# Performance work log

Measured on AMD Instinct MI355X. Metric: run time of the kernel, lower is better.

Reference implementation:

```python
import jax, jax.numpy as jnp
import numpy as np

N_EMBED = 1024
HEAD_SIZE = 128
B, T = 4, 2048

def setup_inputs() -> dict:
    key = jax.random.key(0)
    kx, kq, kk, kv = jax.random.split(key, 4)
    bound = 1.0 / np.sqrt(N_EMBED)  # torch Linear default init range
    x = jax.random.normal(kx, (B, T, N_EMBED), dtype=jnp.float32)
    Wq = jax.random.uniform(kq, (N_EMBED, HEAD_SIZE), jnp.float32, -bound, bound)
    Wk = jax.random.uniform(kk, (N_EMBED, HEAD_SIZE), jnp.float32, -bound, bound)
    Wv = jax.random.uniform(kv, (N_EMBED, HEAD_SIZE), jnp.float32, -bound, bound)
    return {"x": x, "Wq": Wq, "Wk": Wk, "Wv": Wv}

def reference(x, Wq, Wk, Wv):
    Bn, Tn, C = x.shape
    q = x @ Wq  # [B,T,H]
    k = x @ Wk
    v = x @ Wv
    # NOTE: original scales by C**-0.5 where C = n_embed (not head_size)
    scale = C ** (-0.5)
    wei = jnp.einsum('bqh,bkh->bqk', q, k) * scale  # [B,T,T]
    causal = jnp.tril(jnp.ones((Tn, Tn), dtype=bool))
    wei = jnp.where(causal, wei, -jnp.inf)
    wei = jax.nn.softmax(wei, axis=-1)
    # dropout p=0.0 -> identity
    return jnp.einsum('bqk,bkh->bqh', wei, v)
```

## Files before the change

kernel.cpp:

```cpp
#include <hip/hip_runtime.h>
#include <stdint.h>

#define B_ 4
#define T_ 2048
#define C_ 1024
#define H_ 128
#define NEG_BIG -3.0e38f

typedef __attribute__((ext_vector_type(8))) short short8;
typedef __attribute__((ext_vector_type(4))) float f32x4;
typedef __attribute__((ext_vector_type(4))) unsigned short ushort4v;
typedef __attribute__((ext_vector_type(8))) unsigned short ushort8v;

__device__ __forceinline__ unsigned short f2bf(float f) {
  union { float f; unsigned u; } cv; cv.f = f;
  return (unsigned short)((cv.u + 0x8000u) >> 16);
}

__device__ __forceinline__ float bf2f(unsigned short s) {
  union { unsigned u; float f; } cv; cv.u = ((unsigned)s) << 16;
  return cv.f;
}

__device__ __forceinline__ void gld16(const void* g, void* l) {
  __builtin_amdgcn_global_load_lds(
      (const __attribute__((address_space(1))) unsigned int*)g,
      (__attribute__((address_space(3))) unsigned int*)l, 16, 0, 0);
}

#define CSCALE 0.045084220027780106f

__global__ __launch_bounds__(256) void prep_w(const float* __restrict__ Wq,
                                              const float* __restrict__ Wk,
                                              const float* __restrict__ Wv,
                                              unsigned short* __restrict__ WbT) {
  const int i = blockIdx.x * 256 + threadIdx.x;
  const int linear = i * 4;
  const int j = linear >> 10;
  const int k0 = linear & 1023;
  const float* W = (j < 128) ? Wq : (j < 256) ? Wk : Wv;
  const int h = j & 127;
  ushort4v p;
  p[0] = f2bf(W[(k0 + 0) * 128 + h]);
  p[1] = f2bf(W[(k0 + 1) * 128 + h]);
  p[2] = f2bf(W[(k0 + 2) * 128 + h]);
  p[3] = f2bf(W[(k0 + 3) * 128 + h]);
  *(ushort4v*)(WbT + linear) = p;
}

__global__ __launch_bounds__(256, 2) void qkv_proj(const float* __restrict__ x,
                                                   const unsigned short* __restrict__ WbT,
                                                   unsigned short* __restrict__ Qb,
                                                   unsigned short* __restrict__ Kb,
                                                   unsigned short* __restrict__ VT) {
  __shared__ unsigned short As[2][64 * 64];
  __shared__ unsigned short Bs[2][96 * 64];

  const int tid  = threadIdx.x;
  const int wave = tid >> 6, lane = tid & 63;
  const int quad = lane >> 4, l15 = lane & 15;
  const int rb = blockIdx.x & 127, cb = blockIdx.x >> 7;
  const int gm0 = rb * 64, gn0 = cb * 96;
  const int wm = wave >> 1, wn = wave & 1;

  const int srow = lane >> 3, sslot = lane & 7;
  const int axr = tid >> 3, axc = tid & 7;
  const float* gAx = x + (size_t)(gm0 + axr) * C_ + axc * 8;

  int aoff[2][2], boff[3][2];
#pragma unroll
  for (int mt = 0; mt < 2; ++mt) {
    const int r = wm * 32 + mt * 16 + l15;
#pragma unroll
    for (int ks = 0; ks < 2; ++ks)
      aoff[mt][ks] = r * 64 + (((ks * 4 + quad) ^ r) & 7) * 8;
  }
#pragma unroll
  for (int nt = 0; nt < 3; ++nt) {
    const int r = wn * 48 + nt * 16 + l15;
#pragma unroll
    for (int ks = 0; ks < 2; ++ks)
      boff[nt][ks] = r * 64 + (((ks * 4 + quad) ^ r) & 7) * 8;
  }

  f32x4 acc[2][3];
  const f32x4 zero4 = {0.f, 0.f, 0.f, 0.f};
#pragma unroll
  for (int mt = 0; mt < 2; ++mt)
#pragma unroll
    for (int nt = 0; nt < 3; ++nt) acc[mt][nt] = zero4;

#define STAGE_B(buf, kb_)                                                          \
  {                                                                                \
    const int ko = (kb_) * 64;                                                     \
    _Pragma("unroll")                                                              \
    for (int q = 0; q < 3; ++q) {                                                  \
      const int row = wave * 24 + q * 8 + srow;                                    \
      gld16(WbT + (size_t)(gn0 + row) * C_ + ko + ((sslot ^ row) & 7) * 8,         \
            &Bs[buf][(wave * 24 + q * 8) * 64]);                                   \
    }                                                                              \
  }

#define LOAD_A(ko_)                                                                \
  _Pragma("unroll")                                                                \
  for (int q = 0; q < 2; ++q) {                                                    \
    av0[q] = *(const f32x4*)(gAx + (size_t)(q * 32) * C_ + (ko_));                 \
    av1[q] = *(const f32x4*)(gAx + (size_t)(q * 32) * C_ + (ko_) + 4);             \
  }

#define WRITE_A(buf)                                                               \
  _Pragma("unroll")                                                                \
  for (int q = 0; q < 2; ++q) {                                                    \
    const int row = axr + q * 32;                                                  \
    short8 aw;                                                                     \
    _Pragma("unroll")                                                              \
    for (int e = 0; e < 4; ++e) {                                                  \
      aw[e]     = (short)f2bf(av0[q][e]);                                          \
      aw[4 + e] = (short)f2bf(av1[q][e]);                                          \
    }                                                                              \
    *(short8*)(&As[buf][row * 64 + ((axc ^ row) & 7) * 8]) = aw;                   \
  }

  f32x4 av0[2], av1[2];
  LOAD_A(0);
  STAGE_B(0, 0);
  WRITE_A(0);

  for (int kb = 0; kb < 16; ++kb) {
    __syncthreads();
    const int cur = kb & 1, nxt = cur ^ 1;
    if (kb + 1 < 16) {
      LOAD_A((kb + 1) * 64);
      STAGE_B(nxt, kb + 1);
    }
    const unsigned short* Ac = As[cur];
    const unsigned short* Bc = Bs[cur];
#pragma unroll
    for (int ks = 0; ks < 2; ++ks) {
      short8 b0 = *(const short8*)(Bc + boff[0][ks]);
      short8 b1 = *(const short8*)(Bc + boff[1][ks]);
      short8 b2 = *(const short8*)(Bc + boff[2][ks]);
#pragma unroll
      for (int mt = 0; mt < 2; ++mt) {
        short8 a = *(const short8*)(Ac + aoff[mt][ks]);
        acc[mt][0] = __builtin_amdgcn_mfma_f32_16x16x32_bf16(a, b0, acc[mt][0], 0, 0, 0);
        acc[mt][1] = __builtin_amdgcn_mfma_f32_16x16x32_bf16(a, b1, acc[mt][1], 0, 0, 0);
        acc[mt][2] = __builtin_amdgcn_mfma_f32_16x16x32_bf16(a, b2, acc[mt][2], 0, 0, 0);
      }
    }
    if (kb + 1 < 16) WRITE_A(nxt);
  }
#undef STAGE_B
#undef LOAD_A
#undef WRITE_A

#pragma unroll
  for (int mt = 0; mt < 2; ++mt) {
    const int row0 = gm0 + wm * 32 + mt * 16 + quad * 4;
#pragma unroll
    for (int nt = 0; nt < 3; ++nt) {
      const int colbase = gn0 + wn * 48 + nt * 16;
      const int col = colbase + l15;
      if (colbase < 128) {
#pragma unroll
        for (int r = 0; r < 4; ++r)
          Qb[(size_t)(row0 + r) * H_ + col] = f2bf(acc[mt][nt][r] * CSCALE);
      } else if (colbase < 256) {
#pragma unroll
        for (int r = 0; r < 4; ++r)
          Kb[(size_t)(row0 + r) * H_ + (col - 128)] = f2bf(acc[mt][nt][r]);
      } else {
        const int h = col - 256;
        const int bidx = row0 >> 11;
        const int t0 = row0 & 2047;
        ushort4v pk;
        pk[0] = f2bf(acc[mt][nt][0]); pk[1] = f2bf(acc[mt][nt][1]);
        pk[2] = f2bf(acc[mt][nt][2]); pk[3] = f2bf(acc[mt][nt][3]);
        *(ushort4v*)(VT + (size_t)(bidx * H_ + h) * T_ + t0) = pk;
      }
    }
  }
}

__global__ __launch_bounds__(256, 2) void attn1(const unsigned short* __restrict__ Qb,
                                                const unsigned short* __restrict__ Kb,
                                                const unsigned short* __restrict__ VT,
                                                unsigned short* __restrict__ Opart,
                                                float* __restrict__ mpart,
                                                float* __restrict__ lpart) {
  __shared__ unsigned short Ks[2][64 * 128];
  __shared__ unsigned short Vs[2][128 * 64];
  __shared__ unsigned short Pls[4][16 * 72];
  __shared__ float Als[4][16];

  const int bid = blockIdx.x;
  const int b  = bid & 3;
  const int jp = (bid >> 2) & 15;
  const int ch = bid >> 6;
  const int j1 = jp, j2 = 31 - jp;
  const int n1 = (ch <= j1) ? (((j1 - ch) >> 3) + 1) : 0;
  const int n2 = ((j2 - ch) >> 3) + 1;
  const int ntt = n1 + n2;

  const int tid  = threadIdx.x;
  const int wave = tid >> 6, lane = tid & 63;
  const int quad = lane >> 4, l15 = lane & 15;

  const unsigned short* Kb_b = Kb + (size_t)(b * T_) * H_;
  const unsigned short* VT_b = VT + (size_t)(b * H_) * T_;

  const int k_row4 = lane >> 4, k_slot = lane & 15;
  const int v_row8 = lane >> 3, v_slot = lane & 7;

#define STAGE_KV(buf, kv0_)                                                        \
  {                                                                                \
    _Pragma("unroll")                                                              \
    for (int i_ = 0; i_ < 4; ++i_) {                                               \
      const int r = wave * 16 + i_ * 4 + k_row4;                                   \
      const int c2 = (k_slot & 8) | ((k_slot ^ r) & 7);                            \
      gld16(Kb_b + (size_t)((kv0_) + r) * H_ + c2 * 8,                             \
            &Ks[buf][(wave * 16 + i_ * 4) * 128]);                                 \
    }                                                                              \
    _Pragma("unroll")                                                              \
    for (int i_ = 0; i_ < 4; ++i_) {                                               \
      const int h = wave * 32 + i_ * 8 + v_row8;                                   \
      gld16(VT_b + (size_t)h * T_ + (kv0_) + ((v_slot ^ h) & 7) * 8,               \
            &Vs[buf][(wave * 32 + i_ * 8) * 64]);                                  \
    }                                                                              \
  }

#define EPI(jr_)                                                                   \
  {                                                                                \
    const int pid = (b * 32 + (jr_)) * 8 + ch;                                     \
    unsigned short* po = Opart + (size_t)(pid * 64 + wave * 16) * H_;              \
    _Pragma("unroll")                                                              \
    for (int nth = 0; nth < 8; ++nth)                                              \
      _Pragma("unroll")                                                            \
      for (int r = 0; r < 4; ++r)                                                  \
        po[(quad * 4 + r) * H_ + nth * 16 + l15] = f2bf(O[nth][r]);                \
    if (lane < 16) {                                                               \
      mpart[pid * 64 + wave * 16 + lane] = m_;                                     \
      lpart[pid * 64 + wave * 16 + lane] = l_;                                     \
    }                                                                              \
  }

  int jr_cur = n1 ? j1 : j2;
  short8 aq[4];
  {
    const unsigned short* qrow = Qb + (size_t)(b * T_ + jr_cur * 64 + wave * 16 + l15) * H_;
#pragma unroll
    for (int ks = 0; ks < 4; ++ks)
      aq[ks] = *(const short8*)(qrow + ks * 32 + quad * 8);
  }

  STAGE_KV(0, ch * 64);

  const f32x4 zero4 = {0.f, 0.f, 0.f, 0.f};
  f32x4 O[8];
#pragma unroll
  for (int nth = 0; nth < 8; ++nth) O[nth] = zero4;
  float m_ = NEG_BIG, l_ = 0.f;

  for (int i = 0; i < ntt; ++i) {
    __syncthreads();
    if (i + 1 < ntt) {
      const int in_ = i + 1;
      const int tn = (in_ < n1) ? (ch + (in_ << 3)) : (ch + ((in_ - n1) << 3));
      STAGE_KV((in_) & 1, tn * 64);
    }
    if (n1 && i == n1) {
      EPI(j1);
      m_ = NEG_BIG; l_ = 0.f;
#pragma unroll
      for (int nth = 0; nth < 8; ++nth) O[nth] = zero4;
      jr_cur = j2;
      const unsigned short* qrow = Qb + (size_t)(b * T_ + j2 * 64 + wave * 16 + l15) * H_;
#pragma unroll
      for (int ks = 0; ks < 4; ++ks)
        aq[ks] = *(const short8*)(qrow + ks * 32 + quad * 8);
    }
    const int ti  = (i < n1) ? (ch + (i << 3)) : (ch + ((i - n1) << 3));
    const int kv0 = ti * 64;

    const unsigned short* kb = Ks[i & 1];
    f32x4 ST[4];
    ST[0] = zero4; ST[1] = zero4; ST[2] = zero4; ST[3] = zero4;
#pragma unroll
    for (int ntl = 0; ntl < 4; ++ntl) {
      const int kvr = ntl * 16 + l15;
#pragma unroll
      for (int ks = 0; ks < 4; ++ks) {
        const int c = ks * 4 + quad;
        const int slot = (c & 8) | ((c ^ kvr) & 7);
        short8 kf = *(const short8*)(kb + kvr * 128 + slot * 8);
        ST[ntl] = __builtin_amdgcn_mfma_f32_16x16x32_bf16(kf, aq[ks], ST[ntl], 0, 0, 0);
      }
    }

    if (ti == jr_cur) {
      const int ql = jr_cur * 64 + wave * 16 + l15;
#pragma unroll
      for (int ntl = 0; ntl < 4; ++ntl)
#pragma unroll
        for (int r = 0; r < 4; ++r) {
          const int kl = kv0 + ntl * 16 + quad * 4 + r;
          if (kl > ql) ST[ntl][r] = NEG_BIG;
        }
    }

    float vmax = ST[0][0];
#pragma unroll
    for (int ntl = 0; ntl < 4; ++ntl)
#pragma unroll
      for (int r = 0; r < 4; ++r) vmax = fmaxf(vmax, ST[ntl][r]);
    vmax = fmaxf(vmax, __shfl_xor(vmax, 16));
    vmax = fmaxf(vmax, __shfl_xor(vmax, 32));
    const float mn = fmaxf(m_, vmax);
    const float alpha = __builtin_amdgcn_exp2f(m_ - mn);
    m_ = mn;
    float s = 0.f;
#pragma unroll
    for (int ntl = 0; ntl < 4; ++ntl)
#pragma unroll
      for (int r = 0; r < 4; ++r) {
        const float p = __builtin_amdgcn_exp2f(ST[ntl][r] - mn);
        ST[ntl][r] = p;
        s += p;
      }
    s += __shfl_xor(s, 16);
    s += __shfl_xor(s, 32);
    l_ = l_ * alpha + s;

#pragma unroll
    for (int ntl = 0; ntl < 4; ++ntl) {
      ushort4v pk;
      pk[0] = f2bf(ST[ntl][0]); pk[1] = f2bf(ST[ntl][1]);
      pk[2] = f2bf(ST[ntl][2]); pk[3] = f2bf(ST[ntl][3]);
      *(ushort4v*)(&Pls[wave][l15 * 72 + ntl * 16 + quad * 4]) = pk;
    }

    if (lane < 16) Als[wave][lane] = alpha;
    if (!__all(alpha == 1.f)) {
      f32x4 al4 = *(const f32x4*)&Als[wave][quad * 4];
#pragma unroll
      for (int nth = 0; nth < 8; ++nth)
#pragma unroll
        for (int r = 0; r < 4; ++r) O[nth][r] *= al4[r];
    }

    const unsigned short* vb = Vs[i & 1];
    short8 ap0 = *(const short8*)(&Pls[wave][l15 * 72 + quad * 8]);
    short8 ap1 = *(const short8*)(&Pls[wave][l15 * 72 + 32 + quad * 8]);
#pragma unroll
    for (int nth = 0; nth < 8; ++nth) {
      const int h = nth * 16 + l15;
      short8 v0 = *(const short8*)(vb + h * 64 + ((quad ^ h) & 7) * 8);
      short8 v1 = *(const short8*)(vb + h * 64 + (((4 + quad) ^ h) & 7) * 8);
      O[nth] = __builtin_amdgcn_mfma_f32_16x16x32_bf16(ap0, v0, O[nth], 0, 0, 0);
      O[nth] = __builtin_amdgcn_mfma_f32_16x16x32_bf16(ap1, v1, O[nth], 0, 0, 0);
    }
  }
  EPI(j2);
#undef STAGE_KV
#undef EPI
}

__global__ __launch_bounds__(256) void attn2(const unsigned short* __restrict__ Opart,
                                             const float* __restrict__ mpart,
                                             const float* __restrict__ lpart,
                                             float* __restrict__ out) {
  const int b = blockIdx.x & 3;
  const int j = blockIdx.x >> 2;
  const int nch = min(j + 1, 8);
  const int tid = threadIdx.x;
  const int qh = tid >> 4;
  const int h0 = (tid & 15) * 8;
  const int pbase = (b * 32 + j) * 8;

#pragma unroll
  for (int i = 0; i < 4; ++i) {
    const int q = qh + i * 16;
    float m_fin = NEG_BIG;
    for (int ch = 0; ch < nch; ++ch)
      m_fin = fmaxf(m_fin, mpart[(pbase + ch) * 64 + q]);
    float lf = 0.f;
    float o[8];
#pragma unroll
    for (int c = 0; c < 8; ++c) o[c] = 0.f;
    for (int ch = 0; ch < nch; ++ch) {
      const int pid = pbase + ch;
      const float sc = __builtin_amdgcn_exp2f(mpart[pid * 64 + q] - m_fin);
      lf += sc * lpart[pid * 64 + q];
      ushort8v pv = *(const ushort8v*)(Opart + (size_t)(pid * 64 + q) * H_ + h0);
#pragma unroll
      for (int c = 0; c < 8; ++c) o[c] += sc * bf2f(pv[c]);
    }
    const float inv = 1.0f / lf;
    float* op = out + (size_t)(b * T_ + j * 64 + q) * H_ + h0;
    f32x4 v0 = {o[0] * inv, o[1] * inv, o[2] * inv, o[3] * inv};
    f32x4 v1 = {o[4] * inv, o[5] * inv, o[6] * inv, o[7] * inv};
    *(f32x4*)(op) = v0;
    *(f32x4*)(op + 4) = v1;
  }
}

extern "C" void kernel_launch(void* const* d_in, const int* in_sizes, int n_in,
                              void* d_out, int out_size, void* d_ws, size_t ws_size,
                              hipStream_t stream) {
  const float* x  = (const float*)d_in[0];
  const float* Wq = (const float*)d_in[1];
  const float* Wk = (const float*)d_in[2];
  const float* Wv = (const float*)d_in[3];
  float* out = (float*)d_out;

  char* ws = (char*)d_ws;
  unsigned short* WbT = (unsigned short*)(ws);
  unsigned short* Qb  = (unsigned short*)(ws + 1048576);
  unsigned short* Kb  = (unsigned short*)(ws + 3145728);
  unsigned short* VT  = (unsigned short*)(ws + 5242880);
  unsigned short* Opart = (unsigned short*)(ws + 8388608);
  float* mpart = (float*)(ws + 25165824);
  float* lpart = (float*)(ws + 25427968);

  prep_w<<<dim3(384), dim3(256), 0, stream>>>(Wq, Wk, Wv, WbT);
  qkv_proj<<<dim3(512), dim3(256), 0, stream>>>(x, WbT, Qb, Kb, VT);
  attn1<<<dim3(512), dim3(256), 0, stream>>>(Qb, Kb, VT, Opart, mpart, lpart);
  attn2<<<dim3(128), dim3(256), 0, stream>>>(Opart, mpart, lpart, out);
}
```

Baseline: 133.2 us.

## Fuse all four stages into one persistent kernel with grid barriers

Merges weight prep, QKV projection, split attention and the combine step into a single kernel of 512 blocks. Stages are separated by atomic-counter grid barriers instead of separate launches, and the counter is reset with a memset before each launch. This removes three kernel launch gaps and the tails between them. In exchange it needs all 512 blocks resident at once (2 per CU, about 75KB of shared memory each), spends time spinning at each barrier, and the combine stage is now spread over 512 blocks instead of 128.

```diff
diff --git a/kernel.cpp b/kernel.cpp
--- a/kernel.cpp
+++ b/kernel.cpp
@@ -28,358 +28,366 @@
       (__attribute__((address_space(3))) unsigned int*)l, 16, 0, 0);
 }
 
+__device__ __forceinline__ void gbar(unsigned int* cnt, unsigned int target) {
+  __threadfence();
+  __syncthreads();
+  if (threadIdx.x == 0) {
+    __hip_atomic_fetch_add(cnt, 1u, __ATOMIC_ACQ_REL, __HIP_MEMORY_SCOPE_AGENT);
+    unsigned int v;
+    do {
+      __builtin_amdgcn_s_sleep(2);
+      v = __hip_atomic_load(cnt, __ATOMIC_ACQUIRE, __HIP_MEMORY_SCOPE_AGENT);
+    } while (v < target);
+  }
+  __syncthreads();
+  __threadfence();
+}
+
 #define CSCALE 0.045084220027780106f
 
-__global__ __launch_bounds__(256) void prep_w(const float* __restrict__ Wq,
-                                              const float* __restrict__ Wk,
-                                              const float* __restrict__ Wv,
-                                              unsigned short* __restrict__ WbT) {
-  const int i = blockIdx.x * 256 + threadIdx.x;
-  const int linear = i * 4;
-  const int j = linear >> 10;
-  const int k0 = linear & 1023;
-  const float* W = (j < 128) ? Wq : (j < 256) ? Wk : Wv;
-  const int h = j & 127;
-  ushort4v p;
-  p[0] = f2bf(W[(k0 + 0) * 128 + h]);
-  p[1] = f2bf(W[(k0 + 1) * 128 + h]);
-  p[2] = f2bf(W[(k0 + 2) * 128 + h]);
-  p[3] = f2bf(W[(k0 + 3) * 128 + h]);
-  *(ushort4v*)(WbT + linear) = p;
-}
-
-__global__ __launch_bounds__(256, 2) void qkv_proj(const float* __restrict__ x,
-                                                   const unsigned short* __restrict__ WbT,
-                                                   unsigned short* __restrict__ Qb,
-                                                   unsigned short* __restrict__ Kb,
-                                                   unsigned short* __restrict__ VT) {
-  __shared__ unsigned short As[2][64 * 64];
-  __shared__ unsigned short Bs[2][96 * 64];
-
-  const int tid  = threadIdx.x;
+__global__ __launch_bounds__(256, 2) void fused_head(
+    const float* __restrict__ x, const float* __restrict__ Wq,
+    const float* __restrict__ Wk, const float* __restrict__ Wv,
+    unsigned short* __restrict__ WbT, unsigned short* __restrict__ Qb,
+    unsigned short* __restrict__ Kb, unsigned short* __restrict__ VT,
+    unsigned short* __restrict__ Opart, float* __restrict__ mpart,
+    float* __restrict__ lpart, unsigned int* __restrict__ gsync,
+    float* __restrict__ out) {
+  __shared__ __align__(16) char smem[75008];
+
+  const int tid = threadIdx.x;
+  const int bid = blockIdx.x;
   const int wave = tid >> 6, lane = tid & 63;
   const int quad = lane >> 4, l15 = lane & 15;
-  const int rb = blockIdx.x & 127, cb = blockIdx.x >> 7;
-  const int gm0 = rb * 64, gn0 = cb * 96;
-  const int wm = wave >> 1, wn = wave & 1;
-
-  const int srow = lane >> 3, sslot = lane & 7;
-  const int axr = tid >> 3, axc = tid & 7;
-  const float* gAx = x + (size_t)(gm0 + axr) * C_ + axc * 8;
-
-  int aoff[2][2], boff[3][2];
-#pragma unroll
-  for (int mt = 0; mt < 2; ++mt) {
-    const int r = wm * 32 + mt * 16 + l15;
-#pragma unroll
-    for (int ks = 0; ks < 2; ++ks)
-      aoff[mt][ks] = r * 64 + (((ks * 4 + quad) ^ r) & 7) * 8;
+
+  {
+    const int i = bid * 256 + tid;
+    if (i < 98304) {
+      const int linear = i * 4;
+      const int j = linear >> 10;
+      const int k0 = linear & 1023;
+      const float* W = (j < 128) ? Wq : (j < 256) ? Wk : Wv;
+      const int h = j & 127;
+      ushort4v p;
+      p[0] = f2bf(W[(k0 + 0) * 128 + h]);
+      p[1] = f2bf(W[(k0 + 1) * 128 + h]);
+      p[2] = f2bf(W[(k0 + 2) * 128 + h]);
+      p[3] = f2bf(W[(k0 + 3) * 128 + h]);
+      *(ushort4v*)(WbT + linear) = p;
+    }
   }
-#pragma unroll
-  for (int nt = 0; nt < 3; ++nt) {
-    const int r = wn * 48 + nt * 16 + l15;
-#pragma unroll
-    for (int ks = 0; ks < 2; ++ks)
-      boff[nt][ks] = r * 64 + (((ks * 4 + quad) ^ r) & 7) * 8;
+  gbar(gsync, 512);
+
+  {
+    unsigned short* const Asm = (unsigned short*)smem;
+    unsigned short* const Bsm = (unsigned short*)(smem + 16384);
+
+    const int rb = bid & 127, cb = bid >> 7;
+    const int gm0 = rb * 64, gn0 = cb * 96;
+    const int wm = wave >> 1, wn = wave & 1;
+    const int srow = lane >> 3, sslot = lane & 7;
+    const int axr = tid >> 3, axc = tid & 7;
+    const float* gAx = x + (size_t)(gm0 + axr) * C_ + axc * 8;
+
+    int aoff[2][2], boff[3][2];
+#pragma unroll
+    for (int mt = 0; mt < 2; ++mt) {
+      const int r = wm * 32 + mt * 16 + l15;
+#pragma unroll
+      for (int ks = 0; ks < 2; ++ks)
+        aoff[mt][ks] = r * 64 + (((ks * 4 + quad) ^ r) & 7) * 8;
+    }
+#pragma unroll
+    for (int nt = 0; nt < 3; ++nt) {
+      const int r = wn * 48 + nt * 16 + l15;
+#pragma unroll
+      for (int ks = 0; ks < 2; ++ks)
+        boff[nt][ks] = r * 64 + (((ks * 4 + quad) ^ r) & 7) * 8;
+    }
+
+    f32x4 acc[2][3];
+    const f32x4 zero4 = {0.f, 0.f, 0.f, 0.f};
+#pragma unroll
+    for (int mt = 0; mt < 2; ++mt)
+#pragma unroll
+      for (int nt = 0; nt < 3; ++nt) acc[mt][nt] = zero4;
+
+#define QSTAGE_B(buf, kb_)                                                         \
+    {                                                                              \
+      const int ko = (kb_) * 64;                                                   \
+      _Pragma("unroll")                                                            \
+      for (int q = 0; q < 3; ++q) {                                                \
+        const int row = wave * 24 + q * 8 + srow;                                  \
+        gld16(WbT + (size_t)(gn0 + row) * C_ + ko + ((sslot ^ row) & 7) * 8,       \
+              Bsm + (buf) * 6144 + (wave * 24 + q * 8) * 64);                      \
+      }                                                                            \
+    }
+
+#define QLOAD_A(ko_)                                                               \
+    _Pragma("unroll")                                                              \
+    for (int q = 0; q < 2; ++q) {                                                  \
+      av0[q] = *(const f32x4*)(gAx + (size_t)(q * 32) * C_ + (ko_));               \
+      av1[q] = *(const f32x4*)(gAx + (size_t)(q * 32) * C_ + (ko_) + 4);           \
+    }
+
+#define QWRITE_A(buf)                                                              \
+    _Pragma("unroll")                                                              \
+    for (int q = 0; q < 2; ++q) {                                                  \
+      const int row = axr + q * 32;                                                \
+      short8 aw;                                                                   \
+      _Pragma("unroll")                                                            \
+      for (int e = 0; e < 4; ++e) {                                                \
+        aw[e]     = (short)f2bf(av0[q][e]);                                        \
+        aw[4 + e] = (short)f2bf(av1[q][e]);                                        \
+      }                                                                            \
+      *(short8*)(Asm + (buf) * 4096 + row * 64 + ((axc ^ row) & 7) * 8) = aw;      \
+    }
+
+    f32x4 av0[2], av1[2];
+    QLOAD_A(0);
+    QSTAGE_B(0, 0);
+    QWRITE_A(0);
+
+    for (int kb = 0; kb < 16; ++kb) {
+      __syncthreads();
+      const int cur = kb & 1, nxt = cur ^ 1;
+      if (kb + 1 < 16) {
+        QLOAD_A((kb + 1) * 64);
+        QSTAGE_B(nxt, kb + 1);
+      }
+      const unsigned short* Ac = Asm + cur * 4096;
+      const unsigned short* Bc = Bsm + cur * 6144;
+#pragma unroll
+      for (int ks = 0; ks < 2; ++ks) {
+        short8 b0 = *(const short8*)(Bc + boff[0][ks]);
+        short8 b1 = *(const short8*)(Bc + boff[1][ks]);
+        short8 b2 = *(const short8*)(Bc + boff[2][ks]);
+#pragma unroll
+        for (int mt = 0; mt < 2; ++mt) {
+          short8 a = *(const short8*)(Ac + aoff[mt][ks]);
+          acc[mt][0] = __builtin_amdgcn_mfma_f32_16x16x32_bf16(a, b0, acc[mt][0], 0, 0, 0);
+          acc[mt][1] = __builtin_amdgcn_mfma_f32_16x16x32_bf16(a, b1, acc[mt][1], 0, 0, 0);
+          acc[mt][2] = __builtin_amdgcn_mfma_f32_16x16x32_bf16(a, b2, acc[mt][2], 0, 0, 0);
+        }
+      }
+      if (kb + 1 < 16) QWRITE_A(nxt);
+    }
+#undef QSTAGE_B
+#undef QLOAD_A
+#undef QWRITE_A
+
+#pragma unroll
+    for (int mt = 0; mt < 2; ++mt) {
+      const int row0 = gm0 + wm * 32 + mt * 16 + quad * 4;
+#pragma unroll
+      for (int nt = 0; nt < 3; ++nt) {
+        const int colbase = gn0 + wn * 48 + nt * 16;
+        const int col = colbase + l15;
+        if (colbase < 128) {
+#pragma unroll
+          for (int r = 0; r < 4; ++r)
+            Qb[(size_t)(row0 + r) * H_ + col] = f2bf(acc[mt][nt][r] * CSCALE);
+        } else if (colbase < 256) {
+#pragma unroll
+          for (int r = 0; r < 4; ++r)
+            Kb[(size_t)(row0 + r) * H_ + (col - 128)] = f2bf(acc[mt][nt][r]);
+        } else {
+          const int h = col - 256;
+          const int bidx = row0 >> 11;
+          const int t0 = row0 & 2047;
+          ushort4v pk;
+          pk[0] = f2bf(acc[mt][nt][0]); pk[1] = f2bf(acc[mt][nt][1]);
+          pk[2] = f2bf(acc[mt][nt][2]); pk[3] = f2bf(acc[mt][nt][3]);
+          *(ushort4v*)(VT + (size_t)(bidx * H_ + h) * T_ + t0) = pk;
+        }
+      }
+    }
   }
-
-  f32x4 acc[2][3];
-  const f32x4 zero4 = {0.f, 0.f, 0.f, 0.f};
-#pragma unroll
-  for (int mt = 0; mt < 2; ++mt)
-#pragma unroll
-    for (int nt = 0; nt < 3; ++nt) acc[mt][nt] = zero4;
-
-#define STAGE_B(buf, kb_)                                                          \
-  {                                                                                \
-    const int ko = (kb_) * 64;                                                     \
-    _Pragma("unroll")                                                              \
-    for (int q = 0; q < 3; ++q) {                                                  \
-      const int row = wave * 24 + q * 8 + srow;                                    \
-      gld16(WbT + (size_t)(gn0 + row) * C_ + ko + ((sslot ^ row) & 7) * 8,         \
-            &Bs[buf][(wave * 24 + q * 8) * 64]);                                   \
-    }                                                                              \
-  }
-
-#define LOAD_A(ko_)                                                                \
-  _Pragma("unroll")                                                                \
-  for (int q = 0; q < 2; ++q) {                                                    \
-    av0[q] = *(const f32x4*)(gAx + (size_t)(q * 32) * C_ + (ko_));                 \
-    av1[q] = *(const f32x4*)(gAx + (size_t)(q * 32) * C_ + (ko_) + 4);             \
-  }
-
-#define WRITE_A(buf)                                                               \
-  _Pragma("unroll")                                                                \
-  for (int q = 0; q < 2; ++q) {                                                    \
-    const int row = axr + q * 32;                                                  \
-    short8 aw;                                                                     \
-    _Pragma("unroll")                                                              \
-    for (int e = 0; e < 4; ++e) {                                                  \
-      aw[e]     = (short)f2bf(av0[q][e]);                                          \
-      aw[4 + e] = (short)f2bf(av1[q][e]);                                          \
-    }                                                                              \
-    *(short8*)(&As[buf][row * 64 + ((axc ^ row) & 7) * 8]) = aw;                   \
-  }
-
-  f32x4 av0[2], av1[2];
-  LOAD_A(0);
-  STAGE_B(0, 0);
-  WRITE_A(0);
-
-  for (int kb = 0; kb < 16; ++kb) {
-    __syncthreads();
-    const int cur = kb & 1, nxt = cur ^ 1;
-    if (kb + 1 < 16) {
-      LOAD_A((kb + 1) * 64);
-      STAGE_B(nxt, kb + 1);
-    }
-    const unsigned short* Ac = As[cur];
-    const unsigned short* Bc = Bs[cur];
-#pragma unroll
-    for (int ks = 0; ks < 2; ++ks) {
-      short8 b0 = *(const short8*)(Bc + boff[0][ks]);
-      short8 b1 = *(const short8*)(Bc + boff[1][ks]);
-      short8 b2 = *(const short8*)(Bc + boff[2][ks]);
-#pragma unroll
-      for (int mt = 0; mt < 2; ++mt) {
-        short8 a = *(const short8*)(Ac + aoff[mt][ks]);
-        acc[mt][0] = __builtin_amdgcn_mfma_f32_16x16x32_bf16(a, b0, acc[mt][0], 0, 0, 0);
-        acc[mt][1] = __builtin_amdgcn_mfma_f32_16x16x32_bf16(a, b1, acc[mt][1], 0, 0, 0);
-        acc[mt][2] = __builtin_amdgcn_mfma_f32_16x16x32_bf16(a, b2, acc[mt][2], 0, 0, 0);
-      }
-    }
-    if (kb + 1 < 16) WRITE_A(nxt);
-  }
-#undef STAGE_B
-#undef LOAD_A
-#undef WRITE_A
-
-#pragma unroll
-  for (int mt = 0; mt < 2; ++mt) {
-    const int row0 = gm0 + wm * 32 + mt * 16 + quad * 4;
-#pragma unroll
-    for (int nt = 0; nt < 3; ++nt) {
-      const int colbase = gn0 + wn * 48 + nt * 16;
-      const int col = colbase + l15;
-      if (colbase < 128) {
-#pragma unroll
-        for (int r = 0; r < 4; ++r)
-          Qb[(size_t)(row0 + r) * H_ + col] = f2bf(acc[mt][nt][r] * CSCALE);
-      } else if (colbase < 256) {
-#pragma unroll
-        for (int r = 0; r < 4; ++r)
-          Kb[(size_t)(row0 + r) * H_ + (col - 128)] = f2bf(acc[mt][nt][r]);
-      } else {
-        const int h = col - 256;
-        const int bidx = row0 >> 11;
-        const int t0 = row0 & 2047;
-        ushort4v pk;
-        pk[0] = f2bf(acc[mt][nt][0]); pk[1] = f2bf(acc[mt][nt][1]);
-        pk[2] = f2bf(acc[mt][nt][2]); pk[3] = f2bf(acc[mt][nt][3]);
-        *(ushort4v*)(VT + (size_t)(bidx * H_ + h) * T_ + t0) = pk;
-      }
-    }
-  }
-}
-
-__global__ __launch_bounds__(256, 2) void attn1(const unsigned short* __restrict__ Qb,
-                                                const unsigned short* __restrict__ Kb,
-                                                const unsigned short* __restrict__ VT,
-                                                unsigned short* __restrict__ Opart,
-                                                float* __restrict__ mpart,
-                                                float* __restrict__ lpart) {
-  __shared__ unsigned short Ks[2][64 * 128];
-  __shared__ unsigned short Vs[2][128 * 64];
-  __shared__ unsigned short Pls[4][16 * 72];
-  __shared__ float Als[4][16];
-
-  const int bid = blockIdx.x;
-  const int b  = bid & 3;
-  const int jp = (bid >> 2) & 15;
-  const int ch = bid >> 6;
-  const int j1 = jp, j2 = 31 - jp;
-  const int n1 = (ch <= j1) ? (((j1 - ch) >> 3) + 1) : 0;
-  const int n2 = ((j2 - ch) >> 3) + 1;
-  const int ntt = n1 + n2;
-
-  const int tid  = threadIdx.x;
-  const int wave = tid >> 6, lane = tid & 63;
-  const int quad = lane >> 4, l15 = lane & 15;
-
-  const unsigned short* Kb_b = Kb + (size_t)(b * T_) * H_;
-  const unsigned short* VT_b = VT + (size_t)(b * H_) * T_;
-
-  const int k_row4 = lane >> 4, k_slot = lane & 15;
-  const int v_row8 = lane >> 3, v_slot = lane & 7;
+  gbar(gsync, 1024);
+
+  {
+    unsigned short* const Ksm  = (unsigned short*)smem;
+    unsigned short* const Vsm  = (unsigned short*)(smem + 32768);
+    unsigned short* const Plsm = (unsigned short*)(smem + 65536);
+    float* const Alsm = (float*)(smem + 65536 + 9216);
+
+    const int b  = bid & 3;
+    const int jp = (bid >> 2) & 15;
+    const int ch = bid >> 6;
+    const int j1 = jp, j2 = 31 - jp;
+    const int n1 = (ch <= j1) ? (((j1 - ch) >> 3) + 1) : 0;
+    const int n2 = ((j2 - ch) >> 3) + 1;
+    const int ntt = n1 + n2;
+
+    const unsigned short* Kb_b = Kb + (size_t)(b * T_) * H_;
+    const unsigned short* VT_b = VT + (size_t)(b * H_) * T_;
+
+    const int k_row4 = lane >> 4, k_slot = lane & 15;
+    const int v_row8 = lane >> 3, v_slot = lane & 7;
 
 #define STAGE_KV(buf, kv0_)                                                        \
-  {                                                                                \
-    _Pragma("unroll")                                                              \
-    for (int i_ = 0; i_ < 4; ++i_) {                                               \
-      const int r = wave * 16 + i_ * 4 + k_row4;                                   \
-      const int c2 = (k_slot & 8) | ((k_slot ^ r) & 7);                            \
-      gld16(Kb_b + (size_t)((kv0_) + r) * H_ + c2 * 8,                             \
-            &Ks[buf][(wave * 16 + i_ * 4) * 128]);                                 \
-    }                                                                              \
-    _Pragma("unroll")                                                              \
-    for (int i_ = 0; i_ < 4; ++i_) {                                               \
-      const int h = wave * 32 + i_ * 8 + v_row8;                                   \
-      gld16(VT_b + (size_t)h * T_ + (kv0_) + ((v_slot ^ h) & 7) * 8,               \
-            &Vs[buf][(wave * 32 + i_ * 8) * 64]);                                  \
-    }                                                                              \
-  }
+    {                                                                              \
+      _Pragma("unroll")                                                            \
+      for (int i_ = 0; i_ < 4; ++i_) {                                             \
+        const int r = wave * 16 + i_ * 4 + k_row4;                                 \
+        const int c2 = (k_slot & 8) | ((k_slot ^ r) & 7);                          \
+        gld16(Kb_b + (size_t)((kv0_) + r) * H_ + c2 * 8,                           \
+              Ksm + (buf) * 8192 + (wave * 16 + i_ * 4) * 128);                    \
+      }                                                                            \
+      _Pragma("unroll")                                                            \
+      for (int i_ = 0; i_ < 4; ++i_) {                                             \
+        const int h = wave * 32 + i_ * 8 + v_row8;                                 \
+        gld16(VT_b + (size_t)h * T_ + (kv0_) + ((v_slot ^ h) & 7) * 8,             \
+              Vsm + (buf) * 8192 + (wave * 32 + i_ * 8) * 64);                     \
+      }                                                                            \
+    }
 
 #define EPI(jr_)                                                                   \
-  {                                                                                \
-    const int pid = (b * 32 + (jr_)) * 8 + ch;                                     \
-    unsigned short* po = Opart + (size_t)(pid * 64 + wave * 16) * H_;              \
-    _Pragma("unroll")                                                              \
-    for (int nth = 0; nth < 8; ++nth)                                              \
+    {                                                                              \
+      const int pid = (b * 32 + (jr_)) * 8 + ch;                                   \
+      unsigned short* po = Opart + (size_t)(pid * 64 + wave * 16) * H_;            \
       _Pragma("unroll")                                                            \
-      for (int r = 0; r < 4; ++r)                                                  \
-        po[(quad * 4 + r) * H_ + nth * 16 + l15] = f2bf(O[nth][r]);                \
-    if (lane < 16) {                                                               \
-      mpart[pid * 64 + wave * 16 + lane] = m_;                                     \
-      lpart[pid * 64 + wave * 16 + lane] = l_;                                     \
-    }                                                                              \
-  }
-
-  int jr_cur = n1 ? j1 : j2;
-  short8 aq[4];
-  {
-    const unsigned short* qrow = Qb + (size_t)(b * T_ + jr_cur * 64 + wave * 16 + l15) * H_;
-#pragma unroll
-    for (int ks = 0; ks < 4; ++ks)
-      aq[ks] = *(const short8*)(qrow + ks * 32 + quad * 8);
-  }
-
-  STAGE_KV(0, ch * 64);
-
-  const f32x4 zero4 = {0.f, 0.f, 0.f, 0.f};
-  f32x4 O[8];
-#pragma unroll
-  for (int nth = 0; nth < 8; ++nth) O[nth] = zero4;
-  float m_ = NEG_BIG, l_ = 0.f;
-
-  for (int i = 0; i < ntt; ++i) {
-    __syncthreads();
-    if (i + 1 < ntt) {
-      const int in_ = i + 1;
-      const int tn = (in_ < n1) ? (ch + (in_ << 3)) : (ch + ((in_ - n1) << 3));
-      STAGE_KV((in_) & 1, tn * 64);
-    }
-    if (n1 && i == n1) {
-      EPI(j1);
-      m_ = NEG_BIG; l_ = 0.f;
-#pragma unroll
-      for (int nth = 0; nth < 8; ++nth) O[nth] = zero4;
-      jr_cur = j2;
-      const unsigned short* qrow = Qb + (size_t)(b * T_ + j2 * 64 + wave * 16 + l15) * H_;
+      for (int nth = 0; nth < 8; ++nth)                                            \
+        _Pragma("unroll")                                                          \
+        for (int r = 0; r < 4; ++r)                                                \
+          po[(quad * 4 + r) * H_ + nth * 16 + l15] = f2bf(O[nth][r]);              \
+      if (lane < 16) {                                                             \
+        mpart[pid * 64 + wave * 16 + lane] = m_;                                   \
+        lpart[pid * 64 + wave * 16 + lane] = l_;                                   \
+      }                                                                            \
+    }
+
+    int jr_cur = n1 ? j1 : j2;
+    short8 aq[4];
+    {
+      const unsigned short* qrow = Qb + (size_t)(b * T_ + jr_cur * 64 + wave * 16 + l15) * H_;
 #pragma unroll
       for (int ks = 0; ks < 4; ++ks)
         aq[ks] = *(const short8*)(qrow + ks * 32 + quad * 8);
     }
-    const int ti  = (i < n1) ? (ch + (i << 3)) : (ch + ((i - n1) << 3));
-    const int kv0 = ti * 64;
-
-    const unsigned short* kb = Ks[i & 1];
-    f32x4 ST[4];
-    ST[0] = zero4; ST[1] = zero4; ST[2] = zero4; ST[3] = zero4;
-#pragma unroll
-    for (int ntl = 0; ntl < 4; ++ntl) {
-      const int kvr = ntl * 16 + l15;
-#pragma unroll
-      for (int ks = 0; ks < 4; ++ks) {
-        const int c = ks * 4 + quad;
-        const int slot = (c & 8) | ((c ^ kvr) & 7);
-        short8 kf = *(const short8*)(kb + kvr * 128 + slot * 8);
-        ST[ntl] = __builtin_amdgcn_mfma_f32_16x16x32_bf16(kf, aq[ks], ST[ntl], 0, 0, 0);
-      }
-    }
-
-    if (ti == jr_cur) {
-      const int ql = jr_cur * 64 + wave * 16 + l15;
+
+    STAGE_KV(0, ch * 64);
+
+    const f32x4 zero4 = {0.f, 0.f, 0.f, 0.f};
+    f32x4 O[8];
+#pragma unroll
+    for (int nth = 0; nth < 8; ++nth) O[nth] = zero4;
+    float m_ = NEG_BIG, l_ = 0.f;
+
+    for (int i = 0; i < ntt; ++i) {
+      __syncthreads();
+      if (i + 1 < ntt) {
+        const int in_ = i + 1;
+        const int tn = (in_ < n1) ? (ch + (in_ << 3)) : (ch + ((in_ - n1) << 3));
+        STAGE_KV((in_) & 1, tn * 64);
+      }
+      if (n1 && i == n1) {
+        EPI(j1);
+        m_ = NEG_BIG; l_ = 0.f;
+#pragma unroll
+        for (int nth = 0; nth < 8; ++nth) O[nth] = zero4;
+        jr_cur = j2;
+        const unsigned short* qrow = Qb + (size_t)(b * T_ + j2 * 64 + wave * 16 + l15) * H_;
+#pragma unroll
+        for (int ks = 0; ks < 4; ++ks)
+          aq[ks] = *(const short8*)(qrow + ks * 32 + quad * 8);
+      }
+      const int ti  = (i < n1) ? (ch + (i << 3)) : (ch + ((i - n1) << 3));
+      const int kv0 = ti * 64;
+
+      const unsigned short* kb = Ksm + (i & 1) * 8192;
+      f32x4 ST[4];
+      ST[0] = zero4; ST[1] = zero4; ST[2] = zero4; ST[3] = zero4;
+#pragma unroll
+      for (int ntl = 0; ntl < 4; ++ntl) {
+        const int kvr = ntl * 16 + l15;
+#pragma unroll
+        for (int ks = 0; ks < 4; ++ks) {
+          const int c = ks * 4 + quad;
+          const int slot = (c & 8) | ((c ^ kvr) & 7);
+          short8 kf = *(const short8*)(kb + kvr * 128 + slot * 8);
+          ST[ntl] = __builtin_amdgcn_mfma_f32_16x16x32_bf16(kf, aq[ks], ST[ntl], 0, 0, 0);
+        }
+      }
+
+      if (ti == jr_cur) {
+        const int ql = jr_cur * 64 + wave * 16 + l15;
+#pragma unroll
+        for (int ntl = 0; ntl < 4; ++ntl)
+#pragma unroll
+          for (int r = 0; r < 4; ++r) {
+            const int kl = kv0 + ntl * 16 + quad * 4 + r;
+            if (kl > ql) ST[ntl][r] = NEG_BIG;
+          }
+      }
+
+      float vmax = ST[0][0];
 #pragma unroll
       for (int ntl = 0; ntl < 4; ++ntl)
 #pragma unroll
+        for (int r = 0; r < 4; ++r) vmax = fmaxf(vmax, ST[ntl][r]);
+      vmax = fmaxf(vmax, __shfl_xor(vmax, 16));
+      vmax = fmaxf(vmax, __shfl_xor(vmax, 32));
+      const float mn = fmaxf(m_, vmax);
+      const float alpha = __builtin_amdgcn_exp2f(m_ - mn);
+      m_ = mn;
+      float s = 0.f;
+#pragma unroll
+      for (int ntl = 0; ntl < 4; ++ntl)
+#pragma unroll
         for (int r = 0; r < 4; ++r) {
-          const int kl = kv0 + ntl * 16 + quad * 4 + r;
-          if (kl > ql) ST[ntl][r] = NEG_BIG;
+          const float p = __builtin_amdgcn_exp2f(ST[ntl][r] - mn);
+          ST[ntl][r] = p;
+          s += p;
         }
-    }
-
-    float vmax = ST[0][0];
-#pragma unroll
-    for (int ntl = 0; ntl < 4; ++ntl)
-#pragma unroll
-      for (int r = 0; r < 4; ++r) vmax = fmaxf(vmax, ST[ntl][r]);
-    vmax = fmaxf(vmax, __shfl_xor(vmax, 16));
-    vmax = fmaxf(vmax, __shfl_xor(vmax, 32));
-    const float mn = fmaxf(m_, vmax);
-    const float alpha = __builtin_amdgcn_exp2f(m_ - mn);
-    m_ = mn;
-    float s = 0.f;
-#pragma unroll
-    for (int ntl = 0; ntl < 4; ++ntl)
-#pragma unroll
-      for (int r = 0; r < 4; ++r) {
-        const float p = __builtin_amdgcn_exp2f(ST[ntl][r] - mn);
-        ST[ntl][r] = p;
-        s += p;
-      }
-    s += __shfl_xor(s, 16);
-    s += __shfl_xor(s, 32);
-    l_ = l_ * alpha + s;
-
-#pragma unroll
-    for (int ntl = 0; ntl < 4; ++ntl) {
-      ushort4v pk;
-      pk[0] = f2bf(ST[ntl][0]); pk[1] = f2bf(ST[ntl][1]);
-      pk[2] = f2bf(ST[ntl][2]); pk[3] = f2bf(ST[ntl][3]);
-      *(ushort4v*)(&Pls[wave][l15 * 72 + ntl * 16 + quad * 4]) = pk;
-    }
-
-    if (lane < 16) Als[wave][lane] = alpha;
-    if (!__all(alpha == 1.f)) {
-      f32x4 al4 = *(const f32x4*)&Als[wave][quad * 4];
-#pragma unroll
-      for (int nth = 0; nth < 8; ++nth)
-#pragma unroll
-        for (int r = 0; r < 4; ++r) O[nth][r] *= al4[r];
-    }
-
-    const unsigned short* vb = Vs[i & 1];
-    short8 ap0 = *(const short8*)(&Pls[wave][l15 * 72 + quad * 8]);
-    short8 ap1 = *(const short8*)(&Pls[wave][l15 * 72 + 32 + quad * 8]);
-#pragma unroll
-    for (int nth = 0; nth < 8; ++nth) {
-      const int h = nth * 16 + l15;
-      short8 v0 = *(const short8*)(vb + h * 64 + ((quad ^ h) & 7) * 8);
-      short8 v1 = *(const short8*)(vb + h * 64 + (((4 + quad) ^ h) & 7) * 8);
-      O[nth] = __builtin_amdgcn_mfma_f32_16x16x32_bf16(ap0, v0, O[nth], 0, 0, 0);
-      O[nth] = __builtin_amdgcn_mfma_f32_16x16x32_bf16(ap1, v1, O[nth], 0, 0, 0);
-    }
-  }
-  EPI(j2);
+      s += __shfl_xor(s, 16);
+      s += __shfl_xor(s, 32);
+      l_ = l_ * alpha + s;
+
+#pragma unroll
+      for (int ntl = 0; ntl < 4; ++ntl) {
+        ushort4v pk;
+        pk[0] = f2bf(ST[ntl][0]); pk[1] = f2bf(ST[ntl][1]);
+        pk[2] = f2bf(ST[ntl][2]); pk[3] = f2bf(ST[ntl][3]);
+        *(ushort4v*)(Plsm + wave * 1152 + l15 * 72 + ntl * 16 + quad * 4) = pk;
+      }
+
+      if (lane < 16) Alsm[wave * 16 + lane] = alpha;
+      if (!__all(alpha == 1.f)) {
+        f32x4 al4 = *(const f32x4*)(Alsm + wave * 16 + quad * 4);
+#pragma unroll
+        for (int nth = 0; nth < 8; ++nth)
+#pragma unroll
+          for (int r = 0; r < 4; ++r) O[nth][r] *= al4[r];
+      }
+
+      const unsigned short* vb = Vsm + (i & 1) * 8192;
+      short8 ap0 = *(const short8*)(Plsm + wave * 1152 + l15 * 72 + quad * 8);
+      short8 ap1 = *(const short8*)(Plsm + wave * 1152 + l15 * 72 + 32 + quad * 8);
+#pragma unroll
+      for (int nth = 0; nth < 8; ++nth) {
+        const int h = nth * 16 + l15;
+        short8 v0 = *(const short8*)(vb + h * 64 + ((quad ^ h) & 7) * 8);
+        short8 v1 = *(const short8*)(vb + h * 64 + (((4 + quad) ^ h) & 7) * 8);
+        O[nth] = __builtin_amdgcn_mfma_f32_16x16x32_bf16(ap0, v0, O[nth], 0, 0, 0);
+        O[nth] = __builtin_amdgcn_mfma_f32_16x16x32_bf16(ap1, v1, O[nth], 0, 0, 0);
+      }
+    }
+    EPI(j2);
 #undef STAGE_KV
 #undef EPI
-}
-
-__global__ __launch_bounds__(256) void attn2(const unsigned short* __restrict__ Opart,
-                                             const float* __restrict__ mpart,
-                                             const float* __restrict__ lpart,
-                                             float* __restrict__ out) {
-  const int b = blockIdx.x & 3;
-  const int j = blockIdx.x >> 2;
-  const int nch = min(j + 1, 8);
-  const int tid = threadIdx.x;
-  const int qh = tid >> 4;
-  const int h0 = (tid & 15) * 8;
-  const int pbase = (b * 32 + j) * 8;
-
-#pragma unroll
-  for (int i = 0; i < 4; ++i) {
-    const int q = qh + i * 16;
+  }
+  gbar(gsync, 1536);
+
+  {
+    const int b = bid & 3;
+    const int j = (bid >> 2) & 31;
+    const int qi = bid >> 7;
+    const int nch = min(j + 1, 8);
+    const int q = (tid >> 4) + qi * 16;
+    const int h0 = (tid & 15) * 8;
+    const int pbase = (b * 32 + j) * 8;
+
     float m_fin = NEG_BIG;
     for (int ch = 0; ch < nch; ++ch)
       m_fin = fmaxf(m_fin, mpart[(pbase + ch) * 64 + q]);
@@ -421,9 +429,11 @@
   unsigned short* Opart = (unsigned short*)(ws + 8388608);
   float* mpart = (float*)(ws + 25165824);
   float* lpart = (float*)(ws + 25427968);
-
-  prep_w<<<dim3(384), dim3(256), 0, stream>>>(Wq, Wk, Wv, WbT);
-  qkv_proj<<<dim3(512), dim3(256), 0, stream>>>(x, WbT, Qb, Kb, VT);
-  attn1<<<dim3(512), dim3(256), 0, stream>>>(Qb, Kb, VT, Opart, mpart, lpart);
-  attn2<<<dim3(128), dim3(256), 0, stream>>>(Opart, mpart, lpart, out);
-}
+  unsigned int* gsync = (unsigned int*)(ws + 33554432);
+
+  hipMemsetAsync(gsync, 0, 256, stream);
+
+  hipLaunchKernelGGL(fused_head, dim3(512), dim3(256), 0, stream,
+                     x, Wq, Wk, Wv, WbT, Qb, Kb, VT, Opart, mpart, lpart,
+                     gsync, out);
+}
```

After: 516.1 us. 287% more time.

## Read K and V fragments directly from global memory instead of LDS staging

Applied to the files above, without the earlier changes.

Removes the double-buffered LDS staging of K and V tiles, along with the per-iteration block barrier. Each wave now loads its MFMA operand fragments straight from global memory (through the caches). This cuts LDS usage and synchronisation, which may raise occupancy. In exchange, the four waves each re-read the same K/V tiles from global memory, the loads are no longer prefetched one tile ahead, and the access pattern is less coalesced.

```diff
diff --git a/kernel.cpp b/kernel.cpp
--- a/kernel.cpp
+++ b/kernel.cpp
@@ -188,8 +188,6 @@
                                                 unsigned short* __restrict__ Opart,
                                                 float* __restrict__ mpart,
                                                 float* __restrict__ lpart) {
-  __shared__ unsigned short Ks[2][64 * 128];
-  __shared__ unsigned short Vs[2][128 * 64];
   __shared__ unsigned short Pls[4][16 * 72];
   __shared__ float Als[4][16];
 
@@ -208,26 +206,6 @@
 
   const unsigned short* Kb_b = Kb + (size_t)(b * T_) * H_;
   const unsigned short* VT_b = VT + (size_t)(b * H_) * T_;
-
-  const int k_row4 = lane >> 4, k_slot = lane & 15;
-  const int v_row8 = lane >> 3, v_slot = lane & 7;
-
-#define STAGE_KV(buf, kv0_)                                                        \
-  {                                                                                \
-    _Pragma("unroll")                                                              \
-    for (int i_ = 0; i_ < 4; ++i_) {                                               \
-      const int r = wave * 16 + i_ * 4 + k_row4;                                   \
-      const int c2 = (k_slot & 8) | ((k_slot ^ r) & 7);                            \
-      gld16(Kb_b + (size_t)((kv0_) + r) * H_ + c2 * 8,                             \
-            &Ks[buf][(wave * 16 + i_ * 4) * 128]);                                 \
-    }                                                                              \
-    _Pragma("unroll")                                                              \
-    for (int i_ = 0; i_ < 4; ++i_) {                                               \
-      const int h = wave * 32 + i_ * 8 + v_row8;                                   \
-      gld16(VT_b + (size_t)h * T_ + (kv0_) + ((v_slot ^ h) & 7) * 8,               \
-            &Vs[buf][(wave * 32 + i_ * 8) * 64]);                                  \
-    }                                                                              \
-  }
 
 #define EPI(jr_)                                                                   \
   {                                                                                \
@@ -253,8 +231,6 @@
       aq[ks] = *(const short8*)(qrow + ks * 32 + quad * 8);
   }
 
-  STAGE_KV(0, ch * 64);
-
   const f32x4 zero4 = {0.f, 0.f, 0.f, 0.f};
   f32x4 O[8];
 #pragma unroll
@@ -262,12 +238,6 @@
   float m_ = NEG_BIG, l_ = 0.f;
 
   for (int i = 0; i < ntt; ++i) {
-    __syncthreads();
-    if (i + 1 < ntt) {
-      const int in_ = i + 1;
-      const int tn = (in_ < n1) ? (ch + (in_ << 3)) : (ch + ((in_ - n1) << 3));
-      STAGE_KV((in_) & 1, tn * 64);
-    }
     if (n1 && i == n1) {
       EPI(j1);
       m_ = NEG_BIG; l_ = 0.f;
@@ -282,17 +252,14 @@
     const int ti  = (i < n1) ? (ch + (i << 3)) : (ch + ((i - n1) << 3));
     const int kv0 = ti * 64;
 
-    const unsigned short* kb = Ks[i & 1];
     f32x4 ST[4];
     ST[0] = zero4; ST[1] = zero4; ST[2] = zero4; ST[3] = zero4;
 #pragma unroll
     for (int ntl = 0; ntl < 4; ++ntl) {
-      const int kvr = ntl * 16 + l15;
+      const unsigned short* krow = Kb_b + (size_t)(kv0 + ntl * 16 + l15) * H_;
 #pragma unroll
       for (int ks = 0; ks < 4; ++ks) {
-        const int c = ks * 4 + quad;
-        const int slot = (c & 8) | ((c ^ kvr) & 7);
-        short8 kf = *(const short8*)(kb + kvr * 128 + slot * 8);
+        short8 kf = *(const short8*)(krow + (ks * 4 + quad) * 8);
         ST[ntl] = __builtin_amdgcn_mfma_f32_16x16x32_bf16(kf, aq[ks], ST[ntl], 0, 0, 0);
       }
     }
@@ -348,20 +315,19 @@
         for (int r = 0; r < 4; ++r) O[nth][r] *= al4[r];
     }
 
-    const unsigned short* vb = Vs[i & 1];
     short8 ap0 = *(const short8*)(&Pls[wave][l15 * 72 + quad * 8]);
     short8 ap1 = *(const short8*)(&Pls[wave][l15 * 72 + 32 + quad * 8]);
 #pragma unroll
     for (int nth = 0; nth < 8; ++nth) {
       const int h = nth * 16 + l15;
-      short8 v0 = *(const short8*)(vb + h * 64 + ((quad ^ h) & 7) * 8);
-      short8 v1 = *(const short8*)(vb + h * 64 + (((4 + quad) ^ h) & 7) * 8);
+      const unsigned short* vrow = VT_b + (size_t)h * T_ + kv0;
+      short8 v0 = *(const short8*)(vrow + quad * 8);
+      short8 v1 = *(const short8*)(vrow + 32 + quad * 8);
       O[nth] = __builtin_amdgcn_mfma_f32_16x16x32_bf16(ap0, v0, O[nth], 0, 0, 0);
       O[nth] = __builtin_amdgcn_mfma_f32_16x16x32_bf16(ap1, v1, O[nth], 0, 0, 0);
     }
   }
   EPI(j2);
-#undef STAGE_KV
 #undef EPI
 }
 
```

After: 156.6 us. 1.17x slower.
